# Optimization experiments

Measured on AMD Instinct MI355X. Metric: run time of the kernel, lower is better.

Reference implementation:

```python
import jax, jax.numpy as jnp
import numpy as np
from jax import lax

B, T, IN, H = 32, 512, 512, 512
NUM_LAYERS, NUM_DIR = 2, 2


def _lstm_layer(inputs, Wx, Wh, bx, bh, reverse):
    """inputs: [T,B,D]; Wx: [4H,D]; Wh: [4H,H]; bx,bh: [4H]. Returns (hs [T,B,H], hT, cT)."""
    Tn, Bn, _ = inputs.shape
    Hn = Wh.shape[1]
    # Precompute input-to-hidden projections for all timesteps (one big GEMM).
    xg = jnp.einsum('tbd,gd->tbg', inputs, Wx) + bx + bh  # [T,B,4H]
    if reverse:
        xg = xg[::-1]

    def step(carry, xg_t):
        h, c = carry
        g = xg_t + h @ Wh.T  # [B,4H]
        i, f, gg, o = jnp.split(g, 4, axis=-1)  # PyTorch LSTM gate order i,f,g,o
        i = jax.nn.sigmoid(i)
        f = jax.nn.sigmoid(f)
        gg = jnp.tanh(gg)
        o = jax.nn.sigmoid(o)
        c = f * c + i * gg
        h = o * jnp.tanh(c)
        return (h, c), h

    h0 = jnp.zeros((Bn, Hn), dtype=inputs.dtype)
    (hT, cT), hs = lax.scan(step, (h0, h0), xg)
    if reverse:
        hs = hs[::-1]
    return hs, hT, cT


def setup_inputs() -> dict:
    key = jax.random.key(0)
    ks = jax.random.split(key, 20)
    std = 1.0 / np.sqrt(H)
    u = lambda k, shp: jax.random.uniform(k, shp, jnp.float32, -std, std)
    inp = {
        'x': jax.random.normal(ks[0], (B, T, IN), jnp.float32),
        # layer 0: input dim IN, stacked over 2 directions
        'Wx_l0': u(ks[1], (NUM_DIR, 4 * H, IN)),
        'Wh_l0': u(ks[2], (NUM_DIR, 4 * H, H)),
        'bx_l0': u(ks[3], (NUM_DIR, 4 * H)),
        'bh_l0': u(ks[4], (NUM_DIR, 4 * H)),
        # layer 1: input dim 2H (bidirectional concat)
        'Wx_l1': u(ks[5], (NUM_DIR, 4 * H, NUM_DIR * H)),
        'Wh_l1': u(ks[6], (NUM_DIR, 4 * H, H)),
        'bx_l1': u(ks[7], (NUM_DIR, 4 * H)),
        'bh_l1': u(ks[8], (NUM_DIR, 4 * H)),
    }
    return inp


def reference(x, Wx_l0, Wh_l0, bx_l0, bh_l0, Wx_l1, Wh_l1, bx_l1, bh_l1):
    layer_params = [(Wx_l0, Wh_l0, bx_l0, bh_l0), (Wx_l1, Wh_l1, bx_l1, bh_l1)]
    inputs = jnp.transpose(x, (1, 0, 2))  # [T,B,IN] (batch_first -> time-major)
    h_list, c_list = [], []
    for layer in range(NUM_LAYERS):
        Wx, Wh, bx, bh = layer_params[layer]
        dir_outs = []
        for d in range(NUM_DIR):
            hs, hT, cT = _lstm_layer(inputs, Wx[d], Wh[d], bx[d], bh[d], reverse=(d == 1))
            dir_outs.append(hs)
            h_list.append(hT)
            c_list.append(cT)
        inputs = jnp.concatenate(dir_outs, axis=-1)  # [T,B,2H] (dropout=0.0)
    output = jnp.transpose(inputs, (1, 0, 2))  # [B,T,2H]
    h_n = jnp.stack(h_list)  # [num_layers*num_dir, B, H]
    c_n = jnp.stack(c_list)
    return output, h_n, c_n
```

## Files before the change

### kernel.cpp

```cpp
#include <hip/hip_runtime.h>

typedef _Float16 f16;
typedef _Float16 f16x2 __attribute__((ext_vector_type(2)));
typedef _Float16 f16x4 __attribute__((ext_vector_type(4)));
typedef _Float16 f16x8 __attribute__((ext_vector_type(8)));
typedef float f32x4 __attribute__((ext_vector_type(4)));

#define AS1 __attribute__((address_space(1)))
#define AS3 __attribute__((address_space(3)))

static __device__ __forceinline__ float sigf(float x) { return 1.f / (1.f + __expf(-x)); }
static __device__ __forceinline__ float tanh_f(float x) { return 2.f / (1.f + __expf(-2.f * x)) - 1.f; }

__global__ void f2h_kernel(const float* __restrict__ in, f16* __restrict__ out, int n4) {
  const int i = blockIdx.x * blockDim.x + threadIdx.x;
  if (i >= n4) return;
  const float4 v = ((const float4*)in)[i];
  f16x4 o;
  o[0] = (f16)v.x; o[1] = (f16)v.y; o[2] = (f16)v.z; o[3] = (f16)v.w;
  ((f16x4*)out)[i] = o;
}

__global__ void bias_kernel(const float* __restrict__ a, const float* __restrict__ b,
                            float* __restrict__ o, int n) {
  const int i = blockIdx.x * blockDim.x + threadIdx.x;
  if (i < n) o[i] = a[i] + b[i];
}

__global__ __launch_bounds__(256) void gemm_xg(const f16* __restrict__ A,
                                               const f16* __restrict__ Bt,
                                               const float* __restrict__ bias,
                                               f16* __restrict__ outp, int K) {
  __shared__ f16 As[128 * 64];
  __shared__ f16 Bs[128 * 64];
  const int tid = threadIdx.x;
  const int w = tid >> 6, l = tid & 63;
  const int m0 = blockIdx.x << 7, n0 = blockIdx.y << 7;
  const int wm = w >> 1, wn = w & 1;
  f32x4 acc[4][4] = {};

  const int lr8 = l >> 3, lc8 = l & 7;
  const int gcol = (lc8 ^ lr8) << 3;

  for (int k0 = 0; k0 < K; k0 += 64) {
    __syncthreads();
#pragma unroll
    for (int j = 0; j < 4; ++j) {
      const int i = (w << 2) + j;
      const f16* ga = A + (size_t)(m0 + (i << 3) + lr8) * K + (k0 + gcol);
      __builtin_amdgcn_global_load_lds((const AS1 void*)ga, (AS3 void*)(As + (i << 9)), 16, 0, 0);
      const f16* gb = Bt + (size_t)(n0 + (i << 3) + lr8) * K + (k0 + gcol);
      __builtin_amdgcn_global_load_lds((const AS1 void*)gb, (AS3 void*)(Bs + (i << 9)), 16, 0, 0);
    }
    asm volatile("s_waitcnt vmcnt(0)" ::: "memory");
    __syncthreads();

#pragma unroll
    for (int kk = 0; kk < 2; ++kk) {
      const int cb = (kk << 6) + ((l >> 4) << 4);
      f16x8 af[4], bf[4];
#pragma unroll
      for (int a = 0; a < 4; ++a) {
        const int r = (wm << 6) + (a << 4) + (l & 15);
        af[a] = *(const f16x8*)((const char*)As + r * 128 + (cb ^ ((r & 7) << 4)));
      }
#pragma unroll
      for (int b = 0; b < 4; ++b) {
        const int r = (wn << 6) + (b << 4) + (l & 15);
        bf[b] = *(const f16x8*)((const char*)Bs + r * 128 + (cb ^ ((r & 7) << 4)));
      }
#pragma unroll
      for (int a = 0; a < 4; ++a)
#pragma unroll
        for (int b = 0; b < 4; ++b)
          acc[a][b] = __builtin_amdgcn_mfma_f32_16x16x32_f16(af[a], bf[b], acc[a][b], 0, 0, 0);
    }
  }

#pragma unroll
  for (int b = 0; b < 4; ++b) {
    const int col = n0 + (wn << 6) + (b << 4) + (l & 15);
    const float bv = bias[col];
    f16* ob = outp + (size_t)(col >> 11) * (16384ull * 2048) + (col & 2047);
#pragma unroll
    for (int a = 0; a < 4; ++a) {
      const int row0 = m0 + (wm << 6) + (a << 4) + ((l >> 4) << 2);
#pragma unroll
      for (int r = 0; r < 4; ++r)
        ob[(size_t)(row0 + r) * 2048] = (f16)(acc[a][b][r] + bv);
    }
  }
}

__global__ __launch_bounds__(256) void lstm_scan(const f16* __restrict__ Whb,
                                                 const f16* __restrict__ xg,
                                                 unsigned long long* __restrict__ ring,
                                                 f16* __restrict__ h0_all,
                                                 float* __restrict__ outf,
                                                 float* __restrict__ hn,
                                                 float* __restrict__ cn,
                                                 const int layer) {
  __shared__ f16 Wh_s[64 * 512];
  __shared__ f16 h_s[32 * 512];
  __shared__ float G_s[4 * 32 * 18];

  const int tid = threadIdx.x;
  const int dir = blockIdx.x >> 5;
  const int s = blockIdx.x & 31;
  const int w = tid >> 6, l = tid & 63;

#pragma unroll
  for (int j = 0; j < 16; ++j) {
    const int chunk = (j << 8) + tid;
    const int lr = chunk >> 6;
    const int cbyte = (chunk & 63) << 4;
    const int g = lr >> 4, u = lr & 15;
    const char* src = (const char*)Whb + (((size_t)dir * 2048 + (g << 9) + (s << 4) + u) << 10) + cbyte;
    const uint4 v = *(const uint4*)src;
    *(uint4*)((char*)Wh_s + (lr << 10) + (cbyte ^ ((lr & 7) << 4))) = v;
  }

  unsigned long long* rdir = ring + ((size_t)dir << 15);
  const int bb = tid >> 3;
  const int up = tid & 7;

  float c0 = 0.f, c1 = 0.f;
  __syncthreads();

#pragma unroll 1
  for (int t = 0; t < 512; ++t) {
    const int tau = dir ? (511 - t) : t;
    const f16* xr = xg + (((size_t)dir * 16384 + (size_t)bb * 512 + (size_t)tau) << 11) + (s << 4) + (up << 1);
    const f16x2 xv0 = *(const f16x2*)(xr);
    const f16x2 xv1 = *(const f16x2*)(xr + 512);
    const f16x2 xv2 = *(const f16x2*)(xr + 1024);
    const f16x2 xv3 = *(const f16x2*)(xr + 1536);

    float pi0 = 0.f, pi1 = 0.f, pf0 = 0.f, pf1 = 0.f, pg0 = 0.f, pg1 = 0.f, po0 = 0.f, po1 = 0.f;

    if (t > 0) {
      const unsigned tgt = (unsigned)t;
      const unsigned long long* rs = rdir + ((size_t)(t & 3) << 13);
      unsigned long long v[8][4];
      bool ok[8];
#pragma unroll
      for (int j = 0; j < 8; ++j) ok[j] = false;
      int remaining = 8;
      int guard = 0;
      for (;;) {
#pragma unroll
        for (int j = 0; j < 8; ++j) {
          if (!ok[j]) {
            const int chunk = (j << 8) + tid;
            const unsigned long long* sp = rs + ((chunk >> 6) << 8) + ((chunk & 63) << 2);
#pragma unroll
            for (int q = 0; q < 4; ++q)
              v[j][q] = __hip_atomic_load(sp + q, __ATOMIC_RELAXED, __HIP_MEMORY_SCOPE_AGENT);
          }
        }
#pragma unroll
        for (int j = 0; j < 8; ++j) {
          if (!ok[j]) {
            if (((unsigned)v[j][0] == tgt) & ((unsigned)v[j][1] == tgt) &
                ((unsigned)v[j][2] == tgt) & ((unsigned)v[j][3] == tgt)) {
              ok[j] = true;
              --remaining;
            }
          }
        }
        if (remaining == 0) break;
        if (++guard > (1 << 20)) break;
      }
#pragma unroll
      for (int j = 0; j < 8; ++j) {
        const int chunk = (j << 8) + tid;
        const int b = chunk >> 6;
        uint4 d;
        d.x = (unsigned)(v[j][0] >> 32);
        d.y = (unsigned)(v[j][1] >> 32);
        d.z = (unsigned)(v[j][2] >> 32);
        d.w = (unsigned)(v[j][3] >> 32);
        const int cbyte = (chunk & 63) << 4;
        *(uint4*)((char*)h_s + (b << 10) + (cbyte ^ ((b & 7) << 4))) = d;
      }
      __syncthreads();

      f32x4 acc0 = {}, acc1 = {};
#pragma unroll
      for (int kk = 0; kk < 16; ++kk) {
        const int cb = (kk << 6) + ((l >> 4) << 4);
        const int ra0 = l & 15;
        const int ra1 = 16 + ra0;
        const int rb = (w << 4) + ra0;
        const f16x8 a0 = *(const f16x8*)((const char*)h_s + (ra0 << 10) + (cb ^ ((ra0 & 7) << 4)));
        const f16x8 a1 = *(const f16x8*)((const char*)h_s + (ra1 << 10) + (cb ^ ((ra1 & 7) << 4)));
        const f16x8 bv = *(const f16x8*)((const char*)Wh_s + (rb << 10) + (cb ^ ((rb & 7) << 4)));
        acc0 = __builtin_amdgcn_mfma_f32_16x16x32_f16(a0, bv, acc0, 0, 0, 0);
        acc1 = __builtin_amdgcn_mfma_f32_16x16x32_f16(a1, bv, acc1, 0, 0, 0);
      }
#pragma unroll
      for (int r = 0; r < 4; ++r) {
        const int dr = ((l >> 4) << 2) + r;
        G_s[((w << 5) + dr) * 18 + (l & 15)] = acc0[r];
        G_s[((w << 5) + 16 + dr) * 18 + (l & 15)] = acc1[r];
      }
      __syncthreads();

      const float* gp = G_s + bb * 18 + (up << 1);
      const float2 vi = *(const float2*)(gp);
      const float2 vf = *(const float2*)(gp + 576);
      const float2 vg = *(const float2*)(gp + 1152);
      const float2 vo = *(const float2*)(gp + 1728);
      pi0 = vi.x; pi1 = vi.y; pf0 = vf.x; pf1 = vf.y;
      pg0 = vg.x; pg1 = vg.y; po0 = vo.x; po1 = vo.y;
    }

    pi0 += (float)xv0[0]; pi1 += (float)xv0[1];
    pf0 += (float)xv1[0]; pf1 += (float)xv1[1];
    pg0 += (float)xv2[0]; pg1 += (float)xv2[1];
    po0 += (float)xv3[0]; po1 += (float)xv3[1];

    const float i0 = sigf(pi0), i1 = sigf(pi1);
    const float f0 = sigf(pf0), f1 = sigf(pf1);
    const float g0 = tanh_f(pg0), g1 = tanh_f(pg1);
    const float o0 = sigf(po0), o1 = sigf(po1);
    c0 = f0 * c0 + i0 * g0;
    c1 = f1 * c1 + i1 * g1;
    const float h0v = o0 * tanh_f(c0);
    const float h1v = o1 * tanh_f(c1);

    union { f16x2 h2; unsigned u; } pk;
    pk.h2[0] = (f16)h0v; pk.h2[1] = (f16)h1v;

    {
      const size_t ridx = ((size_t)((t + 1) & 3) << 13) + ((size_t)bb << 8) + (s << 3) + up;
      const unsigned long long pv = ((unsigned long long)pk.u << 32) | (unsigned long long)(t + 1);
      __hip_atomic_store(rdir + ridx, pv, __ATOMIC_RELAXED, __HIP_MEMORY_SCOPE_AGENT);
    }

    const size_t orow = (((size_t)bb * 512 + (size_t)tau) << 10) + ((size_t)dir << 9) + (s << 4) + (up << 1);
    if (layer == 0) {
      *(unsigned*)(h0_all + orow) = pk.u;
    } else {
      *(float2*)(outf + orow) = make_float2(h0v, h1v);
    }
    if (t == 511) {
      const size_t nidx = (((size_t)(layer << 1) + (size_t)dir) << 14) + ((size_t)bb << 9) + (s << 4) + (up << 1);
      *(float2*)(hn + nidx) = make_float2(h0v, h1v);
      *(float2*)(cn + nidx) = make_float2(c0, c1);
    }
  }
}

extern "C" void kernel_launch(void* const* d_in, const int* in_sizes, int n_in,
                              void* d_out, int out_size, void* d_ws, size_t ws_size,
                              hipStream_t stream) {
  const float* x = (const float*)d_in[0];
  const float* Wx0 = (const float*)d_in[1];
  const float* Wh0 = (const float*)d_in[2];
  const float* bx0 = (const float*)d_in[3];
  const float* bh0 = (const float*)d_in[4];
  const float* Wx1 = (const float*)d_in[5];
  const float* Wh1 = (const float*)d_in[6];
  const float* bx1 = (const float*)d_in[7];
  const float* bh1 = (const float*)d_in[8];

  char* ws = (char*)d_ws;
  size_t off = 0;
  auto alloc = [&](size_t b) { char* p = ws + off; off += (b + 255) & ~(size_t)255; return p; };
  f16* xg = (f16*)alloc(2ull * 16384 * 2048 * 2);
  f16* x_h = (f16*)alloc(16384ull * 512 * 2);
  f16* h0a = (f16*)alloc(16384ull * 1024 * 2);
  f16* Wx0h = (f16*)alloc(2ull * 2048 * 512 * 2);
  f16* Wh0h = (f16*)alloc(2ull * 2048 * 512 * 2);
  f16* Wx1h = (f16*)alloc(2ull * 2048 * 1024 * 2);
  f16* Wh1h = (f16*)alloc(2ull * 2048 * 512 * 2);
  float* bias0 = (float*)alloc(4096 * 4);
  float* bias1 = (float*)alloc(4096 * 4);
  unsigned long long* ring0 = (unsigned long long*)alloc(2ull * 4 * 32 * 256 * 8);
  unsigned long long* ring1 = (unsigned long long*)alloc(2ull * 4 * 32 * 256 * 8);
  if (off > ws_size) return;

  float* outp = (float*)d_out;
  float* hn = outp + 16384ull * 1024;
  float* cn = hn + 4ull * 32 * 512;

  hipMemsetAsync(ring0, 0, 2ull * 4 * 32 * 256 * 8, stream);
  hipMemsetAsync(ring1, 0, 2ull * 4 * 32 * 256 * 8, stream);

  f2h_kernel<<<dim3(2097152 / 256), 256, 0, stream>>>(x, x_h, 2097152);
  f2h_kernel<<<dim3(524288 / 256), 256, 0, stream>>>(Wx0, Wx0h, 524288);
  f2h_kernel<<<dim3(524288 / 256), 256, 0, stream>>>(Wh0, Wh0h, 524288);
  f2h_kernel<<<dim3(1048576 / 256), 256, 0, stream>>>(Wx1, Wx1h, 1048576);
  f2h_kernel<<<dim3(524288 / 256), 256, 0, stream>>>(Wh1, Wh1h, 524288);
  bias_kernel<<<16, 256, 0, stream>>>(bx0, bh0, bias0, 4096);
  bias_kernel<<<16, 256, 0, stream>>>(bx1, bh1, bias1, 4096);

  dim3 g(128, 32);
  gemm_xg<<<g, 256, 0, stream>>>(x_h, Wx0h, bias0, xg, 512);
  lstm_scan<<<64, 256, 0, stream>>>(Wh0h, xg, ring0, h0a, nullptr, hn, cn, 0);
  gemm_xg<<<g, 256, 0, stream>>>(h0a, Wx1h, bias1, xg, 1024);
  lstm_scan<<<64, 256, 0, stream>>>(Wh1h, xg, ring1, nullptr, outp, hn, cn, 1);
}
```

Baseline: 5.772 ms.

## Add fast-path mirror ring with XOR-tagged plain loads and remap blocks across XCDs

Each scan step now also writes the hidden state into a mirror ring with a tag formed by XOR-ing the step with the payload. Consumers first poll this mirror with non-atomic sc0 loads for a bounded number of rounds, then fall back to the atomic ring with a per-chunk spin. The kernel also launches 256 blocks, keeps only those with blockIdx&7 in {0,1}, and remaps dir and slice so that each direction's 32 blocks probably share one XCD. The aim is lower cross-block handoff latency through a shared L2. The risks are stale-read retries on the mirror path and an extra store per element.

Result: slower. 8.898 ms (+54.2%).

```diff
diff --git a/kernel.cpp b/kernel.cpp
--- a/kernel.cpp
+++ b/kernel.cpp
@@ -95,6 +95,7 @@
 __global__ __launch_bounds__(256) void lstm_scan(const f16* __restrict__ Whb,
                                                  const f16* __restrict__ xg,
                                                  unsigned long long* __restrict__ ring,
+                                                 unsigned long long* __restrict__ mir,
                                                  f16* __restrict__ h0_all,
                                                  float* __restrict__ outf,
                                                  float* __restrict__ hn,
@@ -104,9 +105,12 @@
   __shared__ f16 h_s[32 * 512];
   __shared__ float G_s[4 * 32 * 18];
 
+  const int xslot = blockIdx.x & 7;
+  if (xslot > 1) return;
+  const int dir = xslot;
+  const int s = blockIdx.x >> 3;
+
   const int tid = threadIdx.x;
-  const int dir = blockIdx.x >> 5;
-  const int s = blockIdx.x & 31;
   const int w = tid >> 6, l = tid & 63;
 
 #pragma unroll
@@ -121,6 +125,7 @@
   }
 
   unsigned long long* rdir = ring + ((size_t)dir << 15);
+  unsigned long long* mdir = mir + ((size_t)dir << 15);
   const int bb = tid >> 3;
   const int up = tid & 7;
 
@@ -140,37 +145,70 @@
 
     if (t > 0) {
       const unsigned tgt = (unsigned)t;
-      const unsigned long long* rs = rdir + ((size_t)(t & 3) << 13);
+      const size_t soff = (size_t)(t & 3) << 13;
+      const unsigned long long* ms = mdir + soff;
+      const unsigned long long* rs = rdir + soff;
       unsigned long long v[8][4];
       bool ok[8];
 #pragma unroll
       for (int j = 0; j < 8; ++j) ok[j] = false;
       int remaining = 8;
-      int guard = 0;
-      for (;;) {
+
+      for (int r = 0; r < 6 && remaining; ++r) {
 #pragma unroll
         for (int j = 0; j < 8; ++j) {
           if (!ok[j]) {
             const int chunk = (j << 8) + tid;
-            const unsigned long long* sp = rs + ((chunk >> 6) << 8) + ((chunk & 63) << 2);
+            const unsigned long long* sp = ms + ((chunk >> 6) << 8) + ((chunk & 63) << 2);
 #pragma unroll
             for (int q = 0; q < 4; ++q)
-              v[j][q] = __hip_atomic_load(sp + q, __ATOMIC_RELAXED, __HIP_MEMORY_SCOPE_AGENT);
+              asm volatile("global_load_dwordx2 %0, %1, off sc0" : "=v"(v[j][q]) : "v"(sp + q));
           }
         }
+        asm volatile("s_waitcnt vmcnt(0)" ::: "memory");
+        __builtin_amdgcn_sched_barrier(0);
 #pragma unroll
         for (int j = 0; j < 8; ++j) {
           if (!ok[j]) {
-            if (((unsigned)v[j][0] == tgt) & ((unsigned)v[j][1] == tgt) &
-                ((unsigned)v[j][2] == tgt) & ((unsigned)v[j][3] == tgt)) {
+            if ((((unsigned)v[j][0] ^ (unsigned)(v[j][0] >> 32)) == tgt) &
+                (((unsigned)v[j][1] ^ (unsigned)(v[j][1] >> 32)) == tgt) &
+                (((unsigned)v[j][2] ^ (unsigned)(v[j][2] >> 32)) == tgt) &
+                (((unsigned)v[j][3] ^ (unsigned)(v[j][3] >> 32)) == tgt)) {
               ok[j] = true;
               --remaining;
             }
           }
         }
-        if (remaining == 0) break;
-        if (++guard > (1 << 20)) break;
-      }
+      }
+
+      if (remaining) {
+#pragma unroll
+        for (int j = 0; j < 8; ++j) {
+          if (!ok[j]) {
+            const int chunk = (j << 8) + tid;
+            const unsigned long long* sp = rs + ((chunk >> 6) << 8) + ((chunk & 63) << 2);
+#pragma unroll
+            for (int q = 0; q < 4; ++q)
+              v[j][q] = __hip_atomic_load(sp + q, __ATOMIC_RELAXED, __HIP_MEMORY_SCOPE_AGENT);
+          }
+        }
+#pragma unroll
+        for (int j = 0; j < 8; ++j) {
+          if (!ok[j]) {
+            const int chunk = (j << 8) + tid;
+            const unsigned long long* sp = rs + ((chunk >> 6) << 8) + ((chunk & 63) << 2);
+            int guard = 0;
+            while (!(((unsigned)v[j][0] == tgt) & ((unsigned)v[j][1] == tgt) &
+                     ((unsigned)v[j][2] == tgt) & ((unsigned)v[j][3] == tgt))) {
+#pragma unroll
+              for (int q = 0; q < 4; ++q)
+                v[j][q] = __hip_atomic_load(sp + q, __ATOMIC_RELAXED, __HIP_MEMORY_SCOPE_AGENT);
+              if (++guard > (1 << 20)) break;
+            }
+          }
+        }
+      }
+
 #pragma unroll
       for (int j = 0; j < 8; ++j) {
         const int chunk = (j << 8) + tid;
@@ -234,6 +272,9 @@
 
     {
       const size_t ridx = ((size_t)((t + 1) & 3) << 13) + ((size_t)bb << 8) + (s << 3) + up;
+      const unsigned long long mv =
+          ((unsigned long long)pk.u << 32) | (unsigned long long)((unsigned)(t + 1) ^ pk.u);
+      mdir[ridx] = mv;
       const unsigned long long pv = ((unsigned long long)pk.u << 32) | (unsigned long long)(t + 1);
       __hip_atomic_store(rdir + ridx, pv, __ATOMIC_RELAXED, __HIP_MEMORY_SCOPE_AGENT);
     }
@@ -277,16 +318,18 @@
   f16* Wh1h = (f16*)alloc(2ull * 2048 * 512 * 2);
   float* bias0 = (float*)alloc(4096 * 4);
   float* bias1 = (float*)alloc(4096 * 4);
-  unsigned long long* ring0 = (unsigned long long*)alloc(2ull * 4 * 32 * 256 * 8);
-  unsigned long long* ring1 = (unsigned long long*)alloc(2ull * 4 * 32 * 256 * 8);
+  const size_t RB = 2ull * 4 * 32 * 256 * 8;
+  unsigned long long* ring0 = (unsigned long long*)alloc(RB);
+  unsigned long long* ring1 = (unsigned long long*)alloc(RB);
+  unsigned long long* mir0 = (unsigned long long*)alloc(RB);
+  unsigned long long* mir1 = (unsigned long long*)alloc(RB);
   if (off > ws_size) return;
 
   float* outp = (float*)d_out;
   float* hn = outp + 16384ull * 1024;
   float* cn = hn + 4ull * 32 * 512;
 
-  hipMemsetAsync(ring0, 0, 2ull * 4 * 32 * 256 * 8, stream);
-  hipMemsetAsync(ring1, 0, 2ull * 4 * 32 * 256 * 8, stream);
+  hipMemsetAsync(ring0, 0, 4 * ((RB + 255) & ~(size_t)255), stream);
 
   f2h_kernel<<<dim3(2097152 / 256), 256, 0, stream>>>(x, x_h, 2097152);
   f2h_kernel<<<dim3(524288 / 256), 256, 0, stream>>>(Wx0, Wx0h, 524288);
@@ -298,7 +341,7 @@
 
   dim3 g(128, 32);
   gemm_xg<<<g, 256, 0, stream>>>(x_h, Wx0h, bias0, xg, 512);
-  lstm_scan<<<64, 256, 0, stream>>>(Wh0h, xg, ring0, h0a, nullptr, hn, cn, 0);
+  lstm_scan<<<256, 256, 0, stream>>>(Wh0h, xg, ring0, mir0, h0a, nullptr, hn, cn, 0);
   gemm_xg<<<g, 256, 0, stream>>>(h0a, Wx1h, bias1, xg, 1024);
-  lstm_scan<<<64, 256, 0, stream>>>(Wh1h, xg, ring1, nullptr, outp, hn, cn, 1);
-}
+  lstm_scan<<<256, 256, 0, stream>>>(Wh1h, xg, ring1, mir1, nullptr, outp, hn, cn, 1);
+}
```
